# Performance work log

Measured on AMD Instinct MI355X. Metric: run time of the kernel, lower is better.

Reference implementation:

```python
import jax, jax.numpy as jnp
import numpy as np

B = 4
S = 1024          # per-sequence length (equal for all sequences)
HQ = 32           # query heads
HK = 8            # kv heads (GQA)
D = 128           # head dim


def setup_inputs() -> dict:
    key = jax.random.key(0)
    k1, k2, k3 = jax.random.split(key, 3)
    total = B * S
    q = jax.random.normal(k1, (total, HQ, D), dtype=jnp.float32)
    k = jax.random.normal(k2, (total, HK, D), dtype=jnp.float32)
    v = jax.random.normal(k3, (total, HK, D), dtype=jnp.float32)
    cu = (jnp.arange(B + 1, dtype=jnp.int32) * S)
    return {
        "q": q, "k": k, "v": v,
        "cu_seqlens_q": cu, "cu_seqlens_k": cu,
        "max_seqlen_q": S, "max_seqlen_k": S,
    }


def reference(q, k, v, cu_seqlens_q, cu_seqlens_k, max_seqlen_q, max_seqlen_k):
    # Varlen causal GQA attention (prefill path of Attention.forward).
    # All sequences have equal length S = max_seqlen_q, so the packed varlen
    # layout is exactly a reshape to (B, S, H, D) -- same math as the
    # per-sequence Python loop in attention_varlen_func.
    total, Hq, Dh = q.shape
    Hk = k.shape[1]
    g = Hq // Hk                      # GQA group size
    Sq = int(max_seqlen_q)
    Bn = total // Sq
    scale = 1.0 / (Dh ** 0.5)

    qb = q.reshape(Bn, Sq, Hk, g, Dh)  # (B,S,Hk,g,D)
    kb = k.reshape(Bn, Sq, Hk, Dh)     # (B,S,Hk,D)
    vb = v.reshape(Bn, Sq, Hk, Dh)

    scores = jnp.einsum('bqhgd,bkhd->bhgqk', qb, kb) * scale  # (B,Hk,g,S,S)
    causal_mask = jnp.triu(jnp.ones((Sq, Sq), dtype=bool), k=1)
    scores = jnp.where(causal_mask, -jnp.inf, scores)
    attn = jax.nn.softmax(scores, axis=-1)
    out = jnp.einsum('bhgqk,bkhd->bqhgd', attn, vb)           # (B,S,Hk,g,D)
    return out.reshape(total, Hq, Dh)
```

## Files before the change

kernel.cpp:

```cpp
#include <hip/hip_runtime.h>
#include <hip/hip_bf16.h>
#include <stdint.h>


typedef __bf16 v8bf __attribute__((ext_vector_type(8)));
typedef __bf16 v4bf __attribute__((ext_vector_type(4)));
typedef float  v16f __attribute__((ext_vector_type(16)));

#define NB  4
#define NS  1024
#define NHQ 32
#define NHK 8
#define ND  128
#define BQ  128
#define BK  64

#define KOFF(r) (16*((r)>>3) + ((((r)>>2)&1)*4) + ((r)&3))

__device__ __forceinline__ int kslot(int row) {
  int o = row & 31;
  return (row >> 5) * 32 + (o & 3) + 4 * ((o >> 3) & 1)
       + 8 * (2 * (o >> 4) + ((o >> 2) & 1));
}

__global__ __launch_bounds__(256)
void prep(const float* __restrict__ kg, const float* __restrict__ vg,
          char* __restrict__ ws)
{
  const int tid = threadIdx.x;
  const int blk = blockIdx.x;
  if (blk < 4096) {
    int gid = blk * 256 + tid;
    int i  = gid & 31;
    int s  = (gid >> 5) & (NS - 1);
    int hk = (gid >> 15) & 7;
    int b  = gid >> 18;
    float4 f = *(const float4*)(kg + ((size_t)((b * NS + s) * NHK + hk)) * ND + 4 * i);
    v4bf kb;
    kb[0]=(__bf16)f.x; kb[1]=(__bf16)f.y; kb[2]=(__bf16)f.z; kb[3]=(__bf16)f.w;
    int t = s >> 6, row = s & 63;
    int slot = kslot(row);
    int byte = (slot * 256 + 8 * i) ^ ((slot & 7) << 4);
    size_t tb = (size_t)((b * 8 + hk) * 16 + t) << 15;
    *(v4bf*)(ws + tb + byte) = kb;
  } else {
    int vid = (blk - 4096) * 256 + tid;
    int d  = vid & 127;
    int g  = (vid >> 7) & 7;
    int t  = (vid >> 10) & 15;
    int hk = (vid >> 14) & 7;
    int b  = vid >> 17;
    const float* vp = vg + ((size_t)((b * NS + t * 64 + g * 8) * NHK + hk)) * ND + d;
    v8bf w;
    #pragma unroll
    for (int e = 0; e < 8; ++e) w[e] = (__bf16)vp[(size_t)e * (NHK * ND)];
    int byte = (d * 8 + (g ^ ((d >> 2) & 7))) * 16;
    size_t tb = (size_t)((b * 8 + hk) * 16 + t) << 15;
    *(v8bf*)(ws + tb + 16384 + byte) = w;
  }
}

__global__ __launch_bounds__(256, 2)
void fattn(const float* __restrict__ qg, const char* __restrict__ kvg,
           float* __restrict__ og)
{
  __shared__ __align__(16) char  KV[2][32768];
  __shared__ __align__(16) float alq[4 * 32];

  const int tid  = threadIdx.x;
  const int lane = tid & 63;
  const int wave = tid >> 6;
  const int half = lane >> 5;
  const int l31  = lane & 31;

  const int bx = blockIdx.x;
  const int hk = bx & 7;
  const int t6 = bx >> 3;
  const int b  = t6 >> 4;
  const int m6 = t6 & 15;
  const int p  = m6 >> 2;
  const int h  = hk * 4 + (m6 & 3);

  const float scale = 0.08838834764831845f;
  const int kvtile = (b * 8 + hk) * 16;

  auto dma = [&](int t_, char* dst) {
    const char* src = kvg + ((size_t)(kvtile + t_) << 15);
    #pragma unroll
    for (int i = 0; i < 8; ++i) {
      int c = wave * 8 + i;
      __builtin_amdgcn_global_load_lds(
        (const __attribute__((address_space(1))) void*)(src + c * 1024 + lane * 16),
        (__attribute__((address_space(3))) void*)(dst + c * 1024),
        16, 0, 0);
    }
  };

  dma(0, KV[0]);
  int cur = 0;

  for (int ph = 0; ph < 2; ++ph) {
    const int qt = ph ? (7 - p) : p;
    const int wv = ph ? (3 - wave) : wave;
    const int q0 = qt * BQ;
    const int wqb = q0 + wv * 32;
    const int qglob = wqb + l31;
    const int ntiles = 2 * (qt + 1);

    v8bf qf[8];
    {
      const float* qp = qg + ((size_t)((b * NS + qglob) * NHQ + h)) * ND + half * 8;
      #pragma unroll
      for (int dM = 0; dM < 8; ++dM) {
        float4 f0 = *(const float4*)(qp + dM * 16);
        float4 f1 = *(const float4*)(qp + dM * 16 + 4);
        v8bf t;
        t[0]=(__bf16)(f0.x*scale); t[1]=(__bf16)(f0.y*scale);
        t[2]=(__bf16)(f0.z*scale); t[3]=(__bf16)(f0.w*scale);
        t[4]=(__bf16)(f1.x*scale); t[5]=(__bf16)(f1.y*scale);
        t[6]=(__bf16)(f1.z*scale); t[7]=(__bf16)(f1.w*scale);
        qf[dM] = t;
      }
    }

    v16f accO[4];
    #pragma unroll
    for (int dt = 0; dt < 4; ++dt)
      #pragma unroll
      for (int e = 0; e < 16; ++e) accO[dt][e] = 0.f;
    float m_run = -INFINITY, l_run = 0.f;

    for (int t = 0; t < ntiles; ++t) {
      const int k0 = t * BK;

      asm volatile("s_waitcnt vmcnt(0)" ::: "memory");
      __syncthreads();

      if (t + 1 < ntiles)      dma(t + 1, KV[cur ^ 1]);
      else if (ph == 0)        dma(0, KV[cur ^ 1]);

      if (k0 <= wqb + 31) {
        const char* ksr = KV[cur];
        const char* vtr = KV[cur] + 16384;
        v16f s0, s1;
        #pragma unroll
        for (int e = 0; e < 16; ++e) { s0[e] = 0.f; s1[e] = 0.f; }
        const int kxor = (l31 & 7) << 4;
        __builtin_amdgcn_s_setprio(1);
        #pragma unroll
        for (int dM = 0; dM < 8; ++dM) {
          v8bf ka = *(const v8bf*)(ksr + ((l31 * 256 + dM * 32 + half * 16) ^ kxor));
          s0 = __builtin_amdgcn_mfma_f32_32x32x16_bf16(ka, qf[dM], s0, 0, 0, 0);
        }
        #pragma unroll
        for (int dM = 0; dM < 8; ++dM) {
          v8bf ka = *(const v8bf*)(ksr + (((32 + l31) * 256 + dM * 32 + half * 16) ^ kxor));
          s1 = __builtin_amdgcn_mfma_f32_32x32x16_bf16(ka, qf[dM], s1, 0, 0, 0);
        }
        __builtin_amdgcn_s_setprio(0);
        if (k0 + BK > wqb) {
          #pragma unroll
          for (int r = 0; r < 16; ++r) {
            int key = k0 + KOFF(r) + half * 8;
            if (key > qglob)      s0[r] = -INFINITY;
            if (key + 32 > qglob) s1[r] = -INFINITY;
          }
        }
        float m0 = s0[0];
        #pragma unroll
        for (int r = 1; r < 16; ++r) m0 = fmaxf(m0, s0[r]);
        #pragma unroll
        for (int r = 0; r < 16; ++r) m0 = fmaxf(m0, s1[r]);
        m0 = fmaxf(m0, __shfl_xor(m0, 32));
        float mn = fmaxf(m_run, m0);
        float rs = 0.f;
        #pragma unroll
        for (int r = 0; r < 16; ++r) { float pp = __expf(s0[r] - mn); s0[r] = pp; rs += pp; }
        #pragma unroll
        for (int r = 0; r < 16; ++r) { float pp = __expf(s1[r] - mn); s1[r] = pp; rs += pp; }
        rs += __shfl_xor(rs, 32);
        if (__any(m0 > m_run)) {
          float al = __expf(m_run - mn);
          if (half == 0) alq[wave * 32 + l31] = al;
          float4 alf[4];
          #pragma unroll
          for (int c = 0; c < 4; ++c)
            alf[c] = *(const float4*)(&alq[wave * 32 + 8 * c + 4 * half]);
          #pragma unroll
          for (int dt = 0; dt < 4; ++dt)
            #pragma unroll
            for (int r = 0; r < 16; ++r)
              accO[dt][r] *= ((const float*)&alf[r >> 2])[r & 3];
          l_run = l_run * al + rs;
        } else {
          l_run += rs;
        }
        m_run = mn;
        __builtin_amdgcn_s_setprio(1);
        #pragma unroll
        for (int C = 0; C < 2; ++C) {
          #pragma unroll
          for (int cp = 0; cp < 2; ++cp) {
            v8bf pf;
            #pragma unroll
            for (int e = 0; e < 8; ++e)
              pf[e] = (__bf16)(C == 0 ? s0[cp * 8 + e] : s1[cp * 8 + e]);
            int g = (C * 2 + cp) * 2 + half;
            #pragma unroll
            for (int dt = 0; dt < 4; ++dt) {
              int d = dt * 32 + l31;
              v8bf vb = *(const v8bf*)(vtr + (d * 8 + (g ^ ((l31 >> 2) & 7))) * 16);
              accO[dt] = __builtin_amdgcn_mfma_f32_32x32x16_bf16(pf, vb, accO[dt], 0, 0, 0);
            }
          }
        }
        __builtin_amdgcn_s_setprio(0);
      }
      cur ^= 1;
    }

    if (half == 0) alq[wave * 32 + l31] = 1.f / l_run;
    float4 invf[4];
    #pragma unroll
    for (int c = 0; c < 4; ++c)
      invf[c] = *(const float4*)(&alq[wave * 32 + 8 * c + 4 * half]);
    #pragma unroll
    for (int dt = 0; dt < 4; ++dt) {
      #pragma unroll
      for (int r = 0; r < 16; ++r) {
        int qrow = (r & 3) + 8 * (r >> 2) + 4 * half;
        float* op = og + ((size_t)((b * NS + wqb + qrow) * NHQ + h)) * ND;
        op[dt * 32 + l31] = accO[dt][r] * ((const float*)&invf[r >> 2])[r & 3];
      }
    }
  }
}

extern "C" void kernel_launch(void* const* d_in, const int* in_sizes, int n_in,
                              void* d_out, int out_size, void* d_ws, size_t ws_size,
                              hipStream_t stream) {
  const float* q = (const float*)d_in[0];
  const float* k = (const float*)d_in[1];
  const float* v = (const float*)d_in[2];
  float* out = (float*)d_out;
  char* ws = (char*)d_ws;
  prep<<<dim3(4096 + 2048), 256, 0, stream>>>(k, v, ws);
  fattn<<<dim3(NB * NHQ * 4), 256, 0, stream>>>(q, ws, out);
}
```

Measured before the change: 190.7 us.

## Load K fragments directly from global memory in MFMA-ready layout, stage only V in LDS

```diff
diff --git a/kernel.cpp b/kernel.cpp
--- a/kernel.cpp
+++ b/kernel.cpp
@@ -14,14 +14,9 @@
 #define ND  128
 #define BQ  128
 #define BK  64
+#define VOFF (8u << 20)
 
 #define KOFF(r) (16*((r)>>3) + ((((r)>>2)&1)*4) + ((r)&3))
-
-__device__ __forceinline__ int kslot(int row) {
-  int o = row & 31;
-  return (row >> 5) * 32 + (o & 3) + 4 * ((o >> 3) & 1)
-       + 8 * (2 * (o >> 4) + ((o >> 2) & 1));
-}
 
 __global__ __launch_bounds__(256)
 void prep(const float* __restrict__ kg, const float* __restrict__ vg,
@@ -38,10 +33,15 @@
     float4 f = *(const float4*)(kg + ((size_t)((b * NS + s) * NHK + hk)) * ND + 4 * i);
     v4bf kb;
     kb[0]=(__bf16)f.x; kb[1]=(__bf16)f.y; kb[2]=(__bf16)f.z; kb[3]=(__bf16)f.w;
-    int t = s >> 6, row = s & 63;
-    int slot = kslot(row);
-    int byte = (slot * 256 + 8 * i) ^ ((slot & 7) << 4);
-    size_t tb = (size_t)((b * 8 + hk) * 16 + t) << 15;
+    int t  = s >> 6;
+    int c  = (s >> 5) & 1;
+    int kk = s & 31;
+    int mu = (kk & 3) + 4 * ((kk >> 3) & 1)
+           + 8 * (2 * ((kk >> 4) & 1) + ((kk >> 2) & 1));
+    int fidx  = c * 8 + (i >> 2);
+    int halfb = (i >> 1) & 1;
+    int byte  = fidx * 1024 + halfb * 512 + mu * 16 + ((4 * i) & 7) * 2;
+    size_t tb = (size_t)((b * 8 + hk) * 16 + t) << 14;
     *(v4bf*)(ws + tb + byte) = kb;
   } else {
     int vid = (blk - 4096) * 256 + tid;
@@ -54,9 +54,9 @@
     v8bf w;
     #pragma unroll
     for (int e = 0; e < 8; ++e) w[e] = (__bf16)vp[(size_t)e * (NHK * ND)];
-    int byte = (d * 8 + (g ^ ((d >> 2) & 7))) * 16;
-    size_t tb = (size_t)((b * 8 + hk) * 16 + t) << 15;
-    *(v8bf*)(ws + tb + 16384 + byte) = w;
+    int byte = (d * 8 + (g ^ ((d >> 1) & 7))) * 16;
+    size_t tb = (size_t)((b * 8 + hk) * 16 + t) << 14;
+    *(v8bf*)(ws + VOFF + tb + byte) = w;
   }
 }
 
@@ -64,7 +64,7 @@
 void fattn(const float* __restrict__ qg, const char* __restrict__ kvg,
            float* __restrict__ og)
 {
-  __shared__ __align__(16) char  KV[2][32768];
+  __shared__ __align__(16) char  Vt[2][16384];
   __shared__ __align__(16) float alq[4 * 32];
 
   const int tid  = threadIdx.x;
@@ -81,14 +81,14 @@
   const int p  = m6 >> 2;
   const int h  = hk * 4 + (m6 & 3);
 
-  const float scale = 0.08838834764831845f;
+  const float scale = 0.12751879523604785f;
   const int kvtile = (b * 8 + hk) * 16;
 
-  auto dma = [&](int t_, char* dst) {
-    const char* src = kvg + ((size_t)(kvtile + t_) << 15);
-    #pragma unroll
-    for (int i = 0; i < 8; ++i) {
-      int c = wave * 8 + i;
+  auto dmaV = [&](int t_, char* dst) {
+    const char* src = kvg + VOFF + ((size_t)(kvtile + t_) << 14);
+    #pragma unroll
+    for (int i = 0; i < 4; ++i) {
+      int c = wave * 4 + i;
       __builtin_amdgcn_global_load_lds(
         (const __attribute__((address_space(1))) void*)(src + c * 1024 + lane * 16),
         (__attribute__((address_space(3))) void*)(dst + c * 1024),
@@ -96,7 +96,7 @@
     }
   };
 
-  dma(0, KV[0]);
+  dmaV(0, Vt[0]);
   int cur = 0;
 
   for (int ph = 0; ph < 2; ++ph) {
@@ -136,27 +136,27 @@
       asm volatile("s_waitcnt vmcnt(0)" ::: "memory");
       __syncthreads();
 
-      if (t + 1 < ntiles)      dma(t + 1, KV[cur ^ 1]);
-      else if (ph == 0)        dma(0, KV[cur ^ 1]);
+      if (t + 1 < ntiles)      dmaV(t + 1, Vt[cur ^ 1]);
+      else if (ph == 0)        dmaV(0, Vt[cur ^ 1]);
 
       if (k0 <= wqb + 31) {
-        const char* ksr = KV[cur];
-        const char* vtr = KV[cur] + 16384;
+        const v8bf* kf = (const v8bf*)(kvg + ((size_t)(kvtile + t) << 14) + lane * 16);
+        v8bf ka0[8], ka1[8];
+        #pragma unroll
+        for (int f = 0; f < 8; ++f) ka0[f] = kf[(size_t)f * 64];
+        #pragma unroll
+        for (int f = 0; f < 8; ++f) ka1[f] = kf[(size_t)(f + 8) * 64];
+
         v16f s0, s1;
         #pragma unroll
         for (int e = 0; e < 16; ++e) { s0[e] = 0.f; s1[e] = 0.f; }
-        const int kxor = (l31 & 7) << 4;
         __builtin_amdgcn_s_setprio(1);
         #pragma unroll
-        for (int dM = 0; dM < 8; ++dM) {
-          v8bf ka = *(const v8bf*)(ksr + ((l31 * 256 + dM * 32 + half * 16) ^ kxor));
-          s0 = __builtin_amdgcn_mfma_f32_32x32x16_bf16(ka, qf[dM], s0, 0, 0, 0);
-        }
-        #pragma unroll
-        for (int dM = 0; dM < 8; ++dM) {
-          v8bf ka = *(const v8bf*)(ksr + (((32 + l31) * 256 + dM * 32 + half * 16) ^ kxor));
-          s1 = __builtin_amdgcn_mfma_f32_32x32x16_bf16(ka, qf[dM], s1, 0, 0, 0);
-        }
+        for (int dM = 0; dM < 8; ++dM)
+          s0 = __builtin_amdgcn_mfma_f32_32x32x16_bf16(ka0[dM], qf[dM], s0, 0, 0, 0);
+        #pragma unroll
+        for (int dM = 0; dM < 8; ++dM)
+          s1 = __builtin_amdgcn_mfma_f32_32x32x16_bf16(ka1[dM], qf[dM], s1, 0, 0, 0);
         __builtin_amdgcn_s_setprio(0);
         if (k0 + BK > wqb) {
           #pragma unroll
@@ -175,12 +175,12 @@
         float mn = fmaxf(m_run, m0);
         float rs = 0.f;
         #pragma unroll
-        for (int r = 0; r < 16; ++r) { float pp = __expf(s0[r] - mn); s0[r] = pp; rs += pp; }
-        #pragma unroll
-        for (int r = 0; r < 16; ++r) { float pp = __expf(s1[r] - mn); s1[r] = pp; rs += pp; }
+        for (int r = 0; r < 16; ++r) { float pp = exp2f(s0[r] - mn); s0[r] = pp; rs += pp; }
+        #pragma unroll
+        for (int r = 0; r < 16; ++r) { float pp = exp2f(s1[r] - mn); s1[r] = pp; rs += pp; }
         rs += __shfl_xor(rs, 32);
         if (__any(m0 > m_run)) {
-          float al = __expf(m_run - mn);
+          float al = exp2f(m_run - mn);
           if (half == 0) alq[wave * 32 + l31] = al;
           float4 alf[4];
           #pragma unroll
@@ -196,6 +196,7 @@
           l_run += rs;
         }
         m_run = mn;
+        const char* vtr = Vt[cur];
         __builtin_amdgcn_s_setprio(1);
         #pragma unroll
         for (int C = 0; C < 2; ++C) {
@@ -209,7 +210,7 @@
             #pragma unroll
             for (int dt = 0; dt < 4; ++dt) {
               int d = dt * 32 + l31;
-              v8bf vb = *(const v8bf*)(vtr + (d * 8 + (g ^ ((l31 >> 2) & 7))) * 16);
+              v8bf vb = *(const v8bf*)(vtr + (d * 8 + (g ^ ((l31 >> 1) & 7))) * 16);
               accO[dt] = __builtin_amdgcn_mfma_f32_32x32x16_bf16(pf, vb, accO[dt], 0, 0, 0);
             }
           }
```

Result: slower. 200.3 us (+5.1%).
